# Kernel optimization log

Measured on AMD Instinct MI355X. Metric: run time of the kernel, lower is better.

## Reference

```python
import jax, jax.numpy as jnp
import numpy as np

NC = 80          # num classes
NL = 3           # num levels
NA = 3           # anchors per level
MAX_DET = 25     # self.maxdetnum
IOU_THRES = 0.7
MAX_WH = 7680.0  # class offset for class-aware NMS (agnostic=False)


def _xywh2xyxy(b):
    cx, cy, w, h = b[..., 0], b[..., 1], b[..., 2], b[..., 3]
    return jnp.stack((cx - w / 2, cy - h / 2, cx + w / 2, cy + h / 2), -1)


def _decode(xi, anchors_i):
    # xi: (bs, na, ny, nx, nc+5) raw logits -> (bs, na*ny*nx, nc+7)
    bs, na, ny, nx, _ = xi.shape
    y = jax.nn.sigmoid(xi)
    yv, xv = jnp.meshgrid(jnp.arange(ny, dtype=xi.dtype),
                          jnp.arange(nx, dtype=xi.dtype), indexing='ij')
    pos = jnp.stack((xv, yv), -1)                    # (ny, nx, 2): (x_col, y_row) grid coords
    xy = y[..., :2] * 2 + (pos - 0.5)                # grid = pos - 0.5 (as in source: xy*2 + grid)
    wh = (y[..., 2:4] * 2) ** 2 * anchors_i[None, :, None, None, :]
    conf = y[..., 4:]                                # obj + nc class probs
    posb = jnp.broadcast_to(pos, xy.shape)
    out = jnp.concatenate((xy, wh, conf, posb), -1)  # (bs, na, ny, nx, nc+7)
    return out.reshape(bs, -1, out.shape[-1])


def _iou_one_vs_all(box, boxes):
    # xyxy IoU of one box vs (N,4) boxes
    lt = jnp.maximum(box[:2], boxes[:, :2])
    rb = jnp.minimum(box[2:], boxes[:, 2:])
    wh = jnp.clip(rb - lt, 0.0)
    inter = wh[:, 0] * wh[:, 1]
    area1 = (box[2] - box[0]) * (box[3] - box[1])
    area2 = (boxes[:, 2] - boxes[:, 0]) * (boxes[:, 3] - boxes[:, 1])
    return inter / (area1 + area2 - inter)


def _nms_image(pred):
    # pred: (N, nc+7). Note: source computes xc = conf>0.25 but never applies it.
    obj = pred[:, 4]
    cls = pred[:, 5:5 + NC] * obj[:, None]           # x[:,5:-2] *= x[:,4:5]
    box = _xywh2xyxy(pred[:, :4])
    conf = cls.max(axis=1)
    j = jnp.argmax(cls, axis=1).astype(pred.dtype)
    det = jnp.concatenate((box, conf[:, None], j[:, None], pred[:, -2:]), axis=1)  # (N, 8)
    order = jnp.argsort(-conf)                       # score-descending (N < max_nms=30000 so cap is no-op)
    det = det[order]
    boxes = det[:, :4] + det[:, 5:6] * MAX_WH        # class-offset boxes
    n = det.shape[0]

    def body(k, carry):
        valid, sel, selv = carry
        has = valid.any()
        idx = jnp.argmax(valid)                      # first unsuppressed = highest remaining score
        iou = _iou_one_vs_all(boxes[idx], boxes)
        valid = valid & (iou <= IOU_THRES)           # self-IoU = 1 > thres removes idx from pool
        sel = sel.at[k].set(idx)
        selv = selv.at[k].set(has)
        return valid, sel, selv

    valid0 = jnp.ones((n,), bool)
    sel0 = jnp.zeros((MAX_DET,), jnp.int32)
    selv0 = jnp.zeros((MAX_DET,), bool)
    _, sel, selv = jax.lax.fori_loop(0, MAX_DET, body, (valid0, sel0, selv0))
    out = det[sel] * selv[:, None].astype(det.dtype)  # pad invalid slots with zeros
    return out, selv


def _level(feature, xi, anchors_i):
    pred = _decode(xi, anchors_i)                    # (bs, N, nc+7)
    dets, selv = jax.vmap(_nms_image)(pred)          # (bs, MAX_DET, 8), (bs, MAX_DET)
    fmap = jnp.transpose(feature, (0, 2, 3, 1))      # (bs, ny, nx, C)
    row = dets[:, :, 7].astype(jnp.int32)            # det[:, -1] = y grid coord -> posX in source
    col = dets[:, :, 6].astype(jnp.int32)            # det[:, -2] = x grid coord -> posY in source
    gathered = jax.vmap(lambda f, r, c: f[r, c])(fmap, row, col)  # (bs, MAX_DET, C)
    return gathered * selv[:, :, None].astype(fmap.dtype)         # rows beyond n_det stay zero


def setup_inputs() -> dict:
    key = jax.random.key(0)
    ks = jax.random.split(key, 7)
    bs = 16
    grids = [(80, 80), (40, 40), (20, 20)]
    chans = [128, 256, 512]
    inp = {}
    for i, ((ny, nx), c) in enumerate(zip(grids, chans)):
        inp[f"x{i}"] = jax.random.normal(ks[i], (bs, NA, ny, nx, NC + 5), jnp.float32)
        inp[f"features{i}"] = jax.random.normal(ks[3 + i], (bs, c, ny, nx), jnp.float32)
    inp["anchors"] = jax.random.uniform(ks[6], (NL, NA, 2), jnp.float32, 1.0, 6.0)
    return inp


def reference(features0, features1, features2, x0, x1, x2, anchors):
    feats = (features0, features1, features2)
    xs = (x0, x1, x2)
    return tuple(_level(feats[i], xs[i], anchors[i]) for i in range(NL))
```

## Files before the change

kernel.cpp:

```cpp
#include <hip/hip_runtime.h>
#include <math.h>
#include <float.h>

#define MAX_DET 25
#define IOU_THRES 0.7f
#define MAX_WH 7680.0f
#define TOPK 256
#define MCAP 512

__device__ __forceinline__ float sigm(float v) {
#pragma clang fp contract(off)
    return 1.0f / (1.0f + expf(-v));
}

template<int NY, int NX>
__device__ __forceinline__ void decode_body(
    int bid, const float* __restrict__ x, const float* __restrict__ anch,
    float* __restrict__ confW, float* __restrict__ boxW)
{
#pragma clang fp contract(off)
    constexpr int HW = NY * NX;
    constexpr int NPC = 3 * HW;
    constexpr int N = 16 * NPC;
    int t = bid * 256 + threadIdx.x;
    int g = t >> 4;
    if (g >= N) return;
    int l16 = t & 15;
    const float* row = x + (long)g * 85;

    float bv = -FLT_MAX; int bc = 0;
#pragma unroll
    for (int j = 0; j < 5; ++j) {
        float v = row[5 + l16 + 16 * j];
        if (v > bv) { bv = v; bc = l16 + 16 * j; }
    }
#pragma unroll
    for (int off = 8; off; off >>= 1) {
        float ov = __shfl_xor(bv, off);
        int   oc = __shfl_xor(bc, off);
        if (ov > bv || (ov == bv && oc < bc)) { bv = ov; bc = oc; }
    }
    if (l16 != 0) return;

    float v0 = row[0], v1 = row[1], v2 = row[2], v3 = row[3], v4 = row[4];
    int i   = g % NPC;
    int a   = i / HW;
    int rem = i - a * HW;
    int gy  = rem / NX;
    int gx  = rem - gy * NX;

    float conf = sigm(bv) * sigm(v4);
    float cx = sigm(v0) * 2.0f + ((float)gx - 0.5f);
    float cy = sigm(v1) * 2.0f + ((float)gy - 0.5f);
    float tw = sigm(v2) * 2.0f, th = sigm(v3) * 2.0f;
    float w = (tw * tw) * anch[a * 2 + 0];
    float h = (th * th) * anch[a * 2 + 1];
    float x1 = cx - w / 2.0f, y1 = cy - h / 2.0f;
    float x2 = cx + w / 2.0f, y2 = cy + h / 2.0f;
    float offc = (float)bc * MAX_WH;

    confW[g] = conf;
    float4 bb = make_float4(x1 + offc, y1 + offc, x2 + offc, y2 + offc);
    *reinterpret_cast<float4*>(boxW + (long)g * 4) = bb;
}

__global__ __launch_bounds__(256) void decode_all_kernel(
    const float* __restrict__ x0, const float* __restrict__ x1, const float* __restrict__ x2,
    const float* __restrict__ anch, float* __restrict__ confW, float* __restrict__ boxW)
{
    int bid = blockIdx.x;
    if (bid < 19200)       decode_body<80, 80>(bid,          x0, anch + 0,  confW,          boxW);
    else if (bid < 24000)  decode_body<40, 40>(bid - 19200,  x1, anch + 6,  confW + 307200, boxW + 307200L * 4);
    else                   decode_body<20, 20>(bid - 24000,  x2, anch + 12, confW + 384000, boxW + 384000L * 4);
}

struct LvlParams {
    const float* feat;
    long candOff;
    long outOff;
    int npc, ny, nx, C;
};

template<int NPC>
__device__ __forceinline__ void run_group(
    const float* __restrict__ gconf, const float* __restrict__ boxW, long base4,
    float* sconf, unsigned long long* sk, unsigned* hist, float (*sbox)[4],
    float (*selBox)[4], int* selIdx, int* selValid, unsigned* wtot ,
    unsigned* misc , int grp, int2* __restrict__ sel)
{
#pragma clang fp contract(off)
    const int tid = threadIdx.x;
    const int lane = tid & 63;
    const int wid = tid >> 6;

    for (int i = tid; i < NPC; i += 1024) sconf[i] = gconf[i];
    if (tid < MAX_DET) selValid[tid] = 0;
    if (tid == 0) misc[0] = 0;
    for (int i = tid; i < MCAP; i += 1024) sk[i] = 0ULL;

    unsigned B = 0, B2 = 0, K2 = 0;
    for (int pass = 0; pass < 2; ++pass) {
        for (int i = tid; i < 2048; i += 1024) hist[i] = 0;
        __syncthreads();
        for (int i = tid; i < NPC; i += 1024) {
            unsigned bits = __float_as_uint(sconf[i]);
            if (pass == 0) atomicAdd(&hist[bits >> 19], 1u);
            else if ((bits >> 19) == B) atomicAdd(&hist[(bits >> 8) & 2047u], 1u);
        }
        __syncthreads();
        unsigned part = hist[tid * 2] + hist[tid * 2 + 1];
        unsigned s = part;
#pragma unroll
        for (int d = 1; d < 64; d <<= 1) {
            unsigned v = __shfl_down(s, d);
            if (lane < 64 - d) s += v;
        }
        if (lane == 0) wtot[wid] = s;
        __syncthreads();
        unsigned S = s;
        for (int w = wid + 1; w < 16; ++w) S += wtot[w];
        unsigned Ktgt = (pass == 0) ? TOPK : K2;
        if (S >= Ktgt && S - part < Ktgt) {
            unsigned acc = S - part;
            for (int i = 1; i >= 0; --i) {
                unsigned h = hist[tid * 2 + i];
                acc += h;
                if (acc >= Ktgt) { misc[2] = (unsigned)(tid * 2 + i); misc[3] = acc - h; break; }
            }
        }
        __syncthreads();
        if (pass == 0) { B = misc[2]; K2 = Ktgt - misc[3]; }
        else           { B2 = misc[2]; }
        __syncthreads();
    }
    unsigned T = (B << 19) | (B2 << 8);

    for (int i = tid; i < NPC; i += 1024) {
        unsigned bits = __float_as_uint(sconf[i]);
        if (bits >= T) {
            unsigned pos = atomicAdd(&misc[0], 1u);
            if (pos < MCAP)
                sk[pos] = ((unsigned long long)bits << 32) | (unsigned)(~i);
        }
    }
    __syncthreads();
    unsigned cn = misc[0];
    int n = (cn < (unsigned)MCAP) ? (int)cn : MCAP;

    for (int ksz = 2; ksz <= MCAP; ksz <<= 1) {
        for (int j = ksz >> 1; j > 0; j >>= 1) {
            for (int i = tid; i < MCAP; i += 1024) {
                int ixj = i ^ j;
                if (ixj > i) {
                    unsigned long long a = sk[i], bb = sk[ixj];
                    bool desc = ((i & ksz) == 0);
                    if (desc ? (a < bb) : (a > bb)) { sk[i] = bb; sk[ixj] = a; }
                }
            }
            __syncthreads();
        }
    }

    if (tid < 256 && tid < n) {
        int idx = (int)(~(unsigned)sk[tid]);
        const float4 bb4 = *reinterpret_cast<const float4*>(boxW + base4 + (long)idx * 4);
        sbox[tid][0] = bb4.x; sbox[tid][1] = bb4.y; sbox[tid][2] = bb4.z; sbox[tid][3] = bb4.w;
    }
    __syncthreads();

    if (tid < 64) {
        int k = 0;
        for (int t = 0; t < n && k < MAX_DET; ++t) {
            float cx1, cy1, cx2, cy2;
            if (t < 256) {
                cx1 = sbox[t][0]; cy1 = sbox[t][1]; cx2 = sbox[t][2]; cy2 = sbox[t][3];
            } else {
                int idx = (int)(~(unsigned)sk[t]);
                const float* bp = boxW + base4 + (long)idx * 4;
                cx1 = bp[0]; cy1 = bp[1]; cx2 = bp[2]; cy2 = bp[3];
            }
            bool rej = false;
            if (tid < k) {
                float sx1 = selBox[tid][0], sy1 = selBox[tid][1];
                float sx2 = selBox[tid][2], sy2 = selBox[tid][3];
                float ltx = fmaxf(sx1, cx1), lty = fmaxf(sy1, cy1);
                float rbx = fminf(sx2, cx2), rby = fminf(sy2, cy2);
                float ww = fmaxf(rbx - ltx, 0.0f), hh = fmaxf(rby - lty, 0.0f);
                float inter = ww * hh;
                float area1 = (sx2 - sx1) * (sy2 - sy1);
                float area2 = (cx2 - cx1) * (cy2 - cy1);
                float iou = inter / (area1 + area2 - inter);
                rej = iou > IOU_THRES;
            }
            rej = __any(rej);
            if (!rej) {
                if (tid == 0) {
                    selIdx[k] = (int)(~(unsigned)sk[t]);
                    selValid[k] = 1;
                    selBox[k][0] = cx1; selBox[k][1] = cy1;
                    selBox[k][2] = cx2; selBox[k][3] = cy2;
                }
                k++;
            }
        }
    }
    __syncthreads();

    if (tid < MAX_DET)
        sel[grp * MAX_DET + tid] = make_int2(selIdx[tid], selValid[tid]);
}

__global__ __launch_bounds__(1024) void select_nms_kernel(
    const float* __restrict__ confW, const float* __restrict__ boxW,
    int2* __restrict__ sel, LvlParams p0, LvlParams p1, LvlParams p2)
{
    __shared__ float sconf[19200];
    __shared__ unsigned long long sk[MCAP];
    __shared__ unsigned hist[2048];
    __shared__ float sbox[256][4];
    __shared__ float selBox[MAX_DET][4];
    __shared__ int   selIdx[MAX_DET];
    __shared__ int   selValid[MAX_DET];
    __shared__ unsigned wtot[16];
    __shared__ unsigned misc[4];

    int grp = blockIdx.x;
    int lvl = grp >> 4, b = grp & 15;
    if (lvl == 0) {
        long base = p0.candOff + (long)b * p0.npc;
        run_group<19200>(confW + base, boxW, base * 4, sconf, sk, hist, sbox, selBox, selIdx, selValid, wtot, misc, grp, sel);
    } else if (lvl == 1) {
        long base = p1.candOff + (long)b * p1.npc;
        run_group<4800>(confW + base, boxW, base * 4, sconf, sk, hist, sbox, selBox, selIdx, selValid, wtot, misc, grp, sel);
    } else {
        long base = p2.candOff + (long)b * p2.npc;
        run_group<1200>(confW + base, boxW, base * 4, sconf, sk, hist, sbox, selBox, selIdx, selValid, wtot, misc, grp, sel);
    }
}

__global__ __launch_bounds__(256) void gather_kernel(
    const int2* __restrict__ sel, float* __restrict__ out,
    LvlParams p0, LvlParams p1, LvlParams p2)
{
    int bid = blockIdx.x;
    int grp = bid / MAX_DET, k = bid - grp * MAX_DET;
    int lvl = grp >> 4, b = grp & 15;
    LvlParams p = (lvl == 0) ? p0 : ((lvl == 1) ? p1 : p2);
    int2 sv = sel[bid];
    long obase = p.outOff + ((long)b * MAX_DET + k) * p.C;
    const int hw = p.ny * p.nx;
    if (sv.y) {
        int rem = sv.x % hw;
        int gy = rem / p.nx, gx = rem - gy * p.nx;
        const float* f = p.feat + (long)b * p.C * hw + (long)gy * p.nx + gx;
        for (int c = threadIdx.x; c < p.C; c += 256)
            out[obase + c] = f[(long)c * hw];
    } else {
        for (int c = threadIdx.x; c < p.C; c += 256)
            out[obase + c] = 0.0f;
    }
}

extern "C" void kernel_launch(void* const* d_in, const int* in_sizes, int n_in,
                              void* d_out, int out_size, void* d_ws, size_t ws_size,
                              hipStream_t stream)
{
    const float* xs[3] = {nullptr, nullptr, nullptr};
    const float* fs[3] = {nullptr, nullptr, nullptr};
    const float* anch  = nullptr;
    for (int i = 0; i < n_in; ++i) {
        const float* p = (const float*)d_in[i];
        switch (in_sizes[i]) {
            case 26112000: xs[0] = p; break;
            case 6528000:  xs[1] = p; break;
            case 1632000:  xs[2] = p; break;
            case 13107200: fs[0] = p; break;
            case 6553600:  fs[1] = p; break;
            case 3276800:  fs[2] = p; break;
            case 18:       anch  = p; break;
        }
    }

    char* wsb = (char*)d_ws;
    float* confW = (float*)wsb;
    float* boxW  = (float*)(wsb + 1612800L);
    int2*  sel   = (int2*)(wsb + 8064000L);

    decode_all_kernel<<<25200, 256, 0, stream>>>(xs[0], xs[1], xs[2], anch, confW, boxW);

    LvlParams P0{fs[0], 0L,      0L,      19200, 80, 80, 128};
    LvlParams P1{fs[1], 307200L, 51200L,  4800,  40, 40, 256};
    LvlParams P2{fs[2], 384000L, 153600L, 1200,  20, 20, 512};

    select_nms_kernel<<<48, 1024, 0, stream>>>(confW, boxW, sel, P0, P1, P2);
    gather_kernel<<<48 * MAX_DET, 256, 0, stream>>>(sel, (float*)d_out, P0, P1, P2);
}
```

Before: 73.71 us.

## Stage decode rows in LDS and replace bitonic sort with lazy wave argmax NMS

```diff
diff --git a/kernel.cpp b/kernel.cpp
--- a/kernel.cpp
+++ b/kernel.cpp
@@ -7,6 +7,9 @@
 #define MAX_WH 7680.0f
 #define TOPK 256
 #define MCAP 512
+#define CPB 64
+#define DEC_F (CPB * 85)
+#define DEC_F4 (DEC_F / 4)
 
 __device__ __forceinline__ float sigm(float v) {
 #pragma clang fp contract(off)
@@ -15,63 +18,77 @@
 
 template<int NY, int NX>
 __device__ __forceinline__ void decode_body(
-    int bid, const float* __restrict__ x, const float* __restrict__ anch,
-    float* __restrict__ confW, float* __restrict__ boxW)
+    int blk, const float* __restrict__ x, const float* __restrict__ anch,
+    float* __restrict__ confW, float* __restrict__ boxW, float* sx)
 {
 #pragma clang fp contract(off)
     constexpr int HW = NY * NX;
     constexpr int NPC = 3 * HW;
-    constexpr int N = 16 * NPC;
-    int t = bid * 256 + threadIdx.x;
-    int g = t >> 4;
-    if (g >= N) return;
-    int l16 = t & 15;
-    const float* row = x + (long)g * 85;
-
-    float bv = -FLT_MAX; int bc = 0;
-#pragma unroll
-    for (int j = 0; j < 5; ++j) {
-        float v = row[5 + l16 + 16 * j];
-        if (v > bv) { bv = v; bc = l16 + 16 * j; }
-    }
-#pragma unroll
-    for (int off = 8; off; off >>= 1) {
-        float ov = __shfl_xor(bv, off);
-        int   oc = __shfl_xor(bc, off);
-        if (ov > bv || (ov == bv && oc < bc)) { bv = ov; bc = oc; }
-    }
-    if (l16 != 0) return;
-
-    float v0 = row[0], v1 = row[1], v2 = row[2], v3 = row[3], v4 = row[4];
-    int i   = g % NPC;
-    int a   = i / HW;
-    int rem = i - a * HW;
-    int gy  = rem / NX;
-    int gx  = rem - gy * NX;
-
-    float conf = sigm(bv) * sigm(v4);
-    float cx = sigm(v0) * 2.0f + ((float)gx - 0.5f);
-    float cy = sigm(v1) * 2.0f + ((float)gy - 0.5f);
-    float tw = sigm(v2) * 2.0f, th = sigm(v3) * 2.0f;
-    float w = (tw * tw) * anch[a * 2 + 0];
-    float h = (th * th) * anch[a * 2 + 1];
-    float x1 = cx - w / 2.0f, y1 = cy - h / 2.0f;
-    float x2 = cx + w / 2.0f, y2 = cy + h / 2.0f;
-    float offc = (float)bc * MAX_WH;
-
-    confW[g] = conf;
-    float4 bb = make_float4(x1 + offc, y1 + offc, x2 + offc, y2 + offc);
-    *reinterpret_cast<float4*>(boxW + (long)g * 4) = bb;
+    const int tid = threadIdx.x;
+
+    const float4* src = (const float4*)(x + (long)blk * DEC_F);
+    float4* dst = (float4*)sx;
+#pragma unroll
+    for (int it = 0; it < 6; ++it) {
+        int i = tid + it * 256;
+        if (i < DEC_F4) dst[i] = src[i];
+    }
+    __syncthreads();
+
+    const int lane = tid & 63, wave = tid >> 6;
+    const int grp = lane >> 4, l16 = lane & 15;
+#pragma unroll
+    for (int r = 0; r < 4; ++r) {
+        int c = wave * 16 + r * 4 + grp;
+        const float* row = sx + c * 85;
+
+        float bv = -FLT_MAX; int bc = 0;
+#pragma unroll
+        for (int j = 0; j < 5; ++j) {
+            float v = row[5 + l16 + 16 * j];
+            if (v > bv) { bv = v; bc = l16 + 16 * j; }
+        }
+#pragma unroll
+        for (int off = 8; off; off >>= 1) {
+            float ov = __shfl_xor(bv, off);
+            int   oc = __shfl_xor(bc, off);
+            if (ov > bv || (ov == bv && oc < bc)) { bv = ov; bc = oc; }
+        }
+        if (l16 == 0) {
+            float v0 = row[0], v1 = row[1], v2 = row[2], v3 = row[3], v4 = row[4];
+            int gl = blk * CPB + c;
+            int i   = gl % NPC;
+            int a   = i / HW;
+            int rem = i - a * HW;
+            int gy  = rem / NX;
+            int gx  = rem - gy * NX;
+
+            float conf = sigm(bv) * sigm(v4);
+            float cx = sigm(v0) * 2.0f + ((float)gx - 0.5f);
+            float cy = sigm(v1) * 2.0f + ((float)gy - 0.5f);
+            float tw = sigm(v2) * 2.0f, th = sigm(v3) * 2.0f;
+            float w = (tw * tw) * anch[a * 2 + 0];
+            float h = (th * th) * anch[a * 2 + 1];
+            float x1 = cx - w / 2.0f, y1 = cy - h / 2.0f;
+            float x2 = cx + w / 2.0f, y2 = cy + h / 2.0f;
+            float offc = (float)bc * MAX_WH;
+
+            confW[gl] = conf;
+            *reinterpret_cast<float4*>(boxW + (long)gl * 4) =
+                make_float4(x1 + offc, y1 + offc, x2 + offc, y2 + offc);
+        }
+    }
 }
 
 __global__ __launch_bounds__(256) void decode_all_kernel(
     const float* __restrict__ x0, const float* __restrict__ x1, const float* __restrict__ x2,
     const float* __restrict__ anch, float* __restrict__ confW, float* __restrict__ boxW)
 {
+    __shared__ float sx[DEC_F];
     int bid = blockIdx.x;
-    if (bid < 19200)       decode_body<80, 80>(bid,          x0, anch + 0,  confW,          boxW);
-    else if (bid < 24000)  decode_body<40, 40>(bid - 19200,  x1, anch + 6,  confW + 307200, boxW + 307200L * 4);
-    else                   decode_body<20, 20>(bid - 24000,  x2, anch + 12, confW + 384000, boxW + 384000L * 4);
+    if (bid < 4800)       decode_body<80, 80>(bid,        x0, anch + 0,  confW,          boxW,              sx);
+    else if (bid < 6000)  decode_body<40, 40>(bid - 4800, x1, anch + 6,  confW + 307200, boxW + 307200L*4,  sx);
+    else                  decode_body<20, 20>(bid - 6000, x2, anch + 12, confW + 384000, boxW + 384000L*4,  sx);
 }
 
 struct LvlParams {
@@ -85,18 +102,19 @@
 __device__ __forceinline__ void run_group(
     const float* __restrict__ gconf, const float* __restrict__ boxW, long base4,
     float* sconf, unsigned long long* sk, unsigned* hist, float (*sbox)[4],
-    float (*selBox)[4], int* selIdx, int* selValid, unsigned* wtot ,
-    unsigned* misc , int grp, int2* __restrict__ sel)
+    int* selIdx, int* selValid, unsigned* wtot , unsigned* misc ,
+    int grp, int2* __restrict__ sel)
 {
 #pragma clang fp contract(off)
     const int tid = threadIdx.x;
     const int lane = tid & 63;
     const int wid = tid >> 6;
 
-    for (int i = tid; i < NPC; i += 1024) sconf[i] = gconf[i];
+    const float4* gc4 = (const float4*)gconf;
+    float4* sc4 = (float4*)sconf;
+    for (int i = tid; i < NPC / 4; i += 1024) sc4[i] = gc4[i];
     if (tid < MAX_DET) selValid[tid] = 0;
     if (tid == 0) misc[0] = 0;
-    for (int i = tid; i < MCAP; i += 1024) sk[i] = 0ULL;
 
     unsigned B = 0, B2 = 0, K2 = 0;
     for (int pass = 0; pass < 2; ++pass) {
@@ -147,60 +165,56 @@
     unsigned cn = misc[0];
     int n = (cn < (unsigned)MCAP) ? (int)cn : MCAP;
 
-    for (int ksz = 2; ksz <= MCAP; ksz <<= 1) {
-        for (int j = ksz >> 1; j > 0; j >>= 1) {
-            for (int i = tid; i < MCAP; i += 1024) {
-                int ixj = i ^ j;
-                if (ixj > i) {
-                    unsigned long long a = sk[i], bb = sk[ixj];
-                    bool desc = ((i & ksz) == 0);
-                    if (desc ? (a < bb) : (a > bb)) { sk[i] = bb; sk[ixj] = a; }
-                }
+    for (int i = tid; i < n; i += 1024) {
+        int idx = (int)(~(unsigned)sk[i]);
+        const float4 bb4 = *reinterpret_cast<const float4*>(boxW + base4 + (long)idx * 4);
+        sbox[i][0] = bb4.x; sbox[i][1] = bb4.y; sbox[i][2] = bb4.z; sbox[i][3] = bb4.w;
+    }
+    __syncthreads();
+
+    if (tid < 64) {
+        unsigned long long kreg[8];
+#pragma unroll
+        for (int j = 0; j < 8; ++j) {
+            int s = tid + 64 * j;
+            kreg[j] = (s < n) ? sk[s] : 0ULL;
+        }
+        float ex1 = 0.f, ey1 = 0.f, ex2 = 0.f, ey2 = 0.f;
+        int k = 0;
+        while (k < MAX_DET) {
+            unsigned long long mk = kreg[0]; int ms = tid;
+#pragma unroll
+            for (int j = 1; j < 8; ++j)
+                if (kreg[j] > mk) { mk = kreg[j]; ms = tid + 64 * j; }
+#pragma unroll
+            for (int off = 32; off; off >>= 1) {
+                unsigned long long ok = __shfl_xor(mk, off);
+                int os = __shfl_xor(ms, off);
+                if (ok > mk) { mk = ok; ms = os; }
             }
-            __syncthreads();
-        }
-    }
-
-    if (tid < 256 && tid < n) {
-        int idx = (int)(~(unsigned)sk[tid]);
-        const float4 bb4 = *reinterpret_cast<const float4*>(boxW + base4 + (long)idx * 4);
-        sbox[tid][0] = bb4.x; sbox[tid][1] = bb4.y; sbox[tid][2] = bb4.z; sbox[tid][3] = bb4.w;
-    }
-    __syncthreads();
-
-    if (tid < 64) {
-        int k = 0;
-        for (int t = 0; t < n && k < MAX_DET; ++t) {
-            float cx1, cy1, cx2, cy2;
-            if (t < 256) {
-                cx1 = sbox[t][0]; cy1 = sbox[t][1]; cx2 = sbox[t][2]; cy2 = sbox[t][3];
-            } else {
-                int idx = (int)(~(unsigned)sk[t]);
-                const float* bp = boxW + base4 + (long)idx * 4;
-                cx1 = bp[0]; cy1 = bp[1]; cx2 = bp[2]; cy2 = bp[3];
-            }
+            if (mk == 0ULL) break;
+#pragma unroll
+            for (int j = 0; j < 8; ++j)
+                if (ms == tid + 64 * j) kreg[j] = 0ULL;
+
+            float cx1 = sbox[ms][0], cy1 = sbox[ms][1];
+            float cx2 = sbox[ms][2], cy2 = sbox[ms][3];
             bool rej = false;
             if (tid < k) {
-                float sx1 = selBox[tid][0], sy1 = selBox[tid][1];
-                float sx2 = selBox[tid][2], sy2 = selBox[tid][3];
-                float ltx = fmaxf(sx1, cx1), lty = fmaxf(sy1, cy1);
-                float rbx = fminf(sx2, cx2), rby = fminf(sy2, cy2);
+                float ltx = fmaxf(ex1, cx1), lty = fmaxf(ey1, cy1);
+                float rbx = fminf(ex2, cx2), rby = fminf(ey2, cy2);
                 float ww = fmaxf(rbx - ltx, 0.0f), hh = fmaxf(rby - lty, 0.0f);
                 float inter = ww * hh;
-                float area1 = (sx2 - sx1) * (sy2 - sy1);
+                float area1 = (ex2 - ex1) * (ey2 - ey1);
                 float area2 = (cx2 - cx1) * (cy2 - cy1);
                 float iou = inter / (area1 + area2 - inter);
                 rej = iou > IOU_THRES;
             }
             rej = __any(rej);
             if (!rej) {
-                if (tid == 0) {
-                    selIdx[k] = (int)(~(unsigned)sk[t]);
-                    selValid[k] = 1;
-                    selBox[k][0] = cx1; selBox[k][1] = cy1;
-                    selBox[k][2] = cx2; selBox[k][3] = cy2;
-                }
-                k++;
+                if (tid == k) { ex1 = cx1; ey1 = cy1; ex2 = cx2; ey2 = cy2; }
+                if (tid == 0) { selIdx[k] = (int)(~(unsigned)mk); selValid[k] = 1; }
+                ++k;
             }
         }
     }
@@ -217,8 +231,7 @@
     __shared__ float sconf[19200];
     __shared__ unsigned long long sk[MCAP];
     __shared__ unsigned hist[2048];
-    __shared__ float sbox[256][4];
-    __shared__ float selBox[MAX_DET][4];
+    __shared__ float sbox[MCAP][4];
     __shared__ int   selIdx[MAX_DET];
     __shared__ int   selValid[MAX_DET];
     __shared__ unsigned wtot[16];
@@ -228,13 +241,13 @@
     int lvl = grp >> 4, b = grp & 15;
     if (lvl == 0) {
         long base = p0.candOff + (long)b * p0.npc;
-        run_group<19200>(confW + base, boxW, base * 4, sconf, sk, hist, sbox, selBox, selIdx, selValid, wtot, misc, grp, sel);
+        run_group<19200>(confW + base, boxW, base * 4, sconf, sk, hist, sbox, selIdx, selValid, wtot, misc, grp, sel);
     } else if (lvl == 1) {
         long base = p1.candOff + (long)b * p1.npc;
-        run_group<4800>(confW + base, boxW, base * 4, sconf, sk, hist, sbox, selBox, selIdx, selValid, wtot, misc, grp, sel);
+        run_group<4800>(confW + base, boxW, base * 4, sconf, sk, hist, sbox, selIdx, selValid, wtot, misc, grp, sel);
     } else {
         long base = p2.candOff + (long)b * p2.npc;
-        run_group<1200>(confW + base, boxW, base * 4, sconf, sk, hist, sbox, selBox, selIdx, selValid, wtot, misc, grp, sel);
+        run_group<1200>(confW + base, boxW, base * 4, sconf, sk, hist, sbox, selIdx, selValid, wtot, misc, grp, sel);
     }
 }
 
@@ -286,7 +299,7 @@
     float* boxW  = (float*)(wsb + 1612800L);
     int2*  sel   = (int2*)(wsb + 8064000L);
 
-    decode_all_kernel<<<25200, 256, 0, stream>>>(xs[0], xs[1], xs[2], anch, confW, boxW);
+    decode_all_kernel<<<6300, 256, 0, stream>>>(xs[0], xs[1], xs[2], anch, confW, boxW);
 
     LvlParams P0{fs[0], 0L,      0L,      19200, 80, 80, 128};
     LvlParams P1{fs[1], 307200L, 51200L,  4800,  40, 40, 256};
```

Result: slower. 83.70 us (+13.6%).
